# Kernel optimization log

Hardware: AMD Instinct MI355X
Metric: run time of the kernel (lower is better)

## Reference

```python
import jax, jax.numpy as jnp
import numpy as np

RANK = 16
ALPHA = 32
SCALE = ALPHA / RANK


def setup_inputs() -> dict:
    key = jax.random.key(0)
    ks = jax.random.split(key, 4)
    B_, S, D, K = 4, 2048, 4096, 4096
    x = jax.random.normal(ks[0], (B_, S, D), dtype=jnp.float32)
    W = jax.random.normal(ks[1], (K, D), dtype=jnp.float32) * 0.02  # torch Linear weight [out,in]
    bias = jax.random.normal(ks[2], (K,), dtype=jnp.float32) * 0.02
    B = jnp.zeros((D, RANK), dtype=jnp.float32)  # LoRA B init to zeros
    A = jax.random.normal(ks[3], (RANK, K), dtype=jnp.float32)
    return {"x": x, "W": W, "bias": bias, "B": B, "A": A}


def reference(x, W, bias, B, A):
    # base linear: x @ W^T + bias
    base = jnp.einsum("bsd,kd->bsk", x, W) + bias
    # low-rank path: scale * (x @ B) @ A
    lora = SCALE * jnp.einsum("bsr,rk->bsk", jnp.einsum("bsd,dr->bsr", x, B), A)
    return base + lora
```

## Files before the change

### kernel.cpp

```cpp
#include <hip/hip_runtime.h>

typedef unsigned short u16;
typedef __attribute__((ext_vector_type(4))) unsigned short u16x4;
typedef __attribute__((ext_vector_type(8))) unsigned short u16x8;
typedef __attribute__((ext_vector_type(8))) short bf16x8;
typedef __attribute__((ext_vector_type(4))) float f32x4;

#define LORA_SCALE 2.0f

__device__ __forceinline__ u16 f2bf(float f) {
  unsigned u = __builtin_bit_cast(unsigned, f);
  u += 0x7FFFu + ((u >> 16) & 1u);
  return (u16)(u >> 16);
}

#define GLOAD16(g, l) __builtin_amdgcn_global_load_lds(                        \
    (const __attribute__((address_space(1))) void*)(g),                        \
    (__attribute__((address_space(3))) void*)(l), 16, 0, 0)

__global__ __launch_bounds__(256) void make_weff(
    const float* __restrict__ W, const float* __restrict__ B,
    const float* __restrict__ A, u16* __restrict__ Wb)
{
  __shared__ float sA[16][64];
  const int n0 = (blockIdx.x >> 4) * 64;
  const int k0 = (blockIdx.x & 15) * 256;
  const int t  = threadIdx.x;

  {
    const int r = t >> 4;
    const int j = (t & 15) * 4;
    const float4 v = *(const float4*)(A + (size_t)r * 4096 + n0 + j);
    sA[r][j + 0] = LORA_SCALE * v.x;
    sA[r][j + 1] = LORA_SCALE * v.y;
    sA[r][j + 2] = LORA_SCALE * v.z;
    sA[r][j + 3] = LORA_SCALE * v.w;
  }
  __syncthreads();

  const int tn = t >> 6;
  const int tk = t & 63;

  float bv[64];
  const float4* pb = (const float4*)(B + (size_t)(k0 + tk * 4) * 16);
#pragma unroll
  for (int q = 0; q < 16; ++q) {
    float4 v = pb[q];
    bv[q * 4 + 0] = v.x; bv[q * 4 + 1] = v.y;
    bv[q * 4 + 2] = v.z; bv[q * 4 + 3] = v.w;
  }

  for (int i = 0; i < 16; ++i) {
    const int n = n0 + tn * 16 + i;
    const float4 w4 = *(const float4*)(W + (size_t)n * 4096 + k0 + tk * 4);
    float acc[4] = {w4.x, w4.y, w4.z, w4.w};
#pragma unroll
    for (int j = 0; j < 4; ++j)
#pragma unroll
      for (int r = 0; r < 16; ++r)
        acc[j] += bv[j * 16 + r] * sA[r][tn * 16 + i];
    u16x4 o;
    o[0] = f2bf(acc[0]); o[1] = f2bf(acc[1]);
    o[2] = f2bf(acc[2]); o[3] = f2bf(acc[3]);
    *(u16x4*)(Wb + (size_t)n * 4096 + k0 + tk * 4) = o;
  }
}

__global__ __launch_bounds__(256) void cvt_x_kernel(
    const float* __restrict__ x, u16* __restrict__ xb, long n)
{
  long i0 = ((long)blockIdx.x * blockDim.x + threadIdx.x) * 8;
  long stride = (long)gridDim.x * blockDim.x * 8;
  for (long i = i0; i < n; i += stride) {
    float4 a = *(const float4*)(x + i);
    float4 b = *(const float4*)(x + i + 4);
    u16x8 o;
    o[0] = f2bf(a.x); o[1] = f2bf(a.y); o[2] = f2bf(a.z); o[3] = f2bf(a.w);
    o[4] = f2bf(b.x); o[5] = f2bf(b.y); o[6] = f2bf(b.z); o[7] = f2bf(b.w);
    *(u16x8*)(xb + i) = o;
  }
}

__global__ __launch_bounds__(512, 2) void gemm256(
    const u16* __restrict__ Xb, const u16* __restrict__ Wb,
    const float* __restrict__ bias, float* __restrict__ out)
{
  constexpr int K = 4096, N = 4096;
  constexpr int NT = K / 32;
  __shared__ char lds[3 * 32768];

  const int t = threadIdx.x;
  const int w = t >> 6, l = t & 63;
  const int wave_m = w >> 2, wave_n = w & 3;

  const int bid = blockIdx.x;
  const int swz = (bid & 7) * 64 + (bid >> 3);
  const int tm = swz >> 4, tn = swz & 15;
  const int m0 = tm * 256, n0 = tn * 256;

  const int lrow = l >> 2;
  const int lch  = ((l & 3) ^ ((l >> 3) & 3)) * 8;
  const u16* gAs = Xb + (size_t)(m0 + w * 16 + lrow) * K + lch;
  const u16* gBs = Wb + (size_t)(n0 + w * 16 + lrow) * K + lch;
  char* ldsw = lds + w * 1024;

#define STAGE_A(tt, bb) do {                                                   \
    GLOAD16(gAs + (size_t)(tt) * 32,                  ldsw + (bb) * 32768);    \
    GLOAD16(gAs + (size_t)(tt) * 32 + 128 * (size_t)K, ldsw + (bb) * 32768 + 8192); \
  } while (0)
#define STAGE_B(tt, bb) do {                                                   \
    GLOAD16(gBs + (size_t)(tt) * 32,                  ldsw + (bb) * 32768 + 16384); \
    GLOAD16(gBs + (size_t)(tt) * 32 + 128 * (size_t)K, ldsw + (bb) * 32768 + 16384 + 8192); \
  } while (0)

  const int fr = l & 15, fq = l >> 4;
  const int coff = (fq ^ ((fr >> 1) & 3)) << 4;
  const char* pa0 = lds + (wave_m * 128 + fr) * 64 + coff;
  const char* pb0 = lds + 16384 + (wave_n * 64 + fr) * 64 + coff;

  f32x4 acc[8][4];
#pragma unroll
  for (int i = 0; i < 8; ++i)
#pragma unroll
    for (int j = 0; j < 4; ++j) acc[i][j] = (f32x4){0.f, 0.f, 0.f, 0.f};

  STAGE_A(0, 0); STAGE_B(0, 0);
  STAGE_A(1, 1); STAGE_B(1, 1);
  asm volatile("s_waitcnt vmcnt(4)" ::: "memory");
  __builtin_amdgcn_s_barrier();

  int b = 0;
  for (int tt = 0; tt < NT; ++tt) {
    const char* pa = pa0 + b * 32768;
    const char* pb = pb0 + b * 32768;
    const int bs = (b == 2) ? 0 : b + 1;
    const int b2 = (b >= 1) ? b - 1 : 2;

    bf16x8 bf[4], af[4];
#pragma unroll
    for (int nj = 0; nj < 4; ++nj)
      bf[nj] = *(const bf16x8*)(pb + nj * 1024);
#pragma unroll
    for (int mi = 0; mi < 4; ++mi)
      af[mi] = *(const bf16x8*)(pa + mi * 1024);
    if (tt + 2 < NT) STAGE_A(tt + 2, b2);
    __builtin_amdgcn_s_setprio(1);
#pragma unroll
    for (int mi = 0; mi < 4; ++mi)
#pragma unroll
      for (int nj = 0; nj < 4; ++nj)
        acc[mi][nj] = __builtin_amdgcn_mfma_f32_16x16x32_bf16(
            af[mi], bf[nj], acc[mi][nj], 0, 0, 0);
    __builtin_amdgcn_s_setprio(0);

#pragma unroll
    for (int mi = 0; mi < 4; ++mi)
      af[mi] = *(const bf16x8*)(pa + 4096 + mi * 1024);
    if (tt + 2 < NT) STAGE_B(tt + 2, b2);
    __builtin_amdgcn_s_setprio(1);
#pragma unroll
    for (int mi = 0; mi < 4; ++mi)
#pragma unroll
      for (int nj = 0; nj < 4; ++nj)
        acc[4 + mi][nj] = __builtin_amdgcn_mfma_f32_16x16x32_bf16(
            af[mi], bf[nj], acc[4 + mi][nj], 0, 0, 0);
    __builtin_amdgcn_s_setprio(0);

    if (tt + 2 < NT) { asm volatile("s_waitcnt vmcnt(4)" ::: "memory"); }
    else             { asm volatile("s_waitcnt vmcnt(0)" ::: "memory"); }
    __builtin_amdgcn_s_barrier();

    b = bs;
  }

  float bvals[4];
#pragma unroll
  for (int nj = 0; nj < 4; ++nj)
    bvals[nj] = bias[n0 + wave_n * 64 + nj * 16 + fr];

#pragma unroll
  for (int ph = 0; ph < 2; ++ph)
#pragma unroll
    for (int mi = 0; mi < 4; ++mi)
#pragma unroll
      for (int i = 0; i < 4; ++i) {
        const int m = m0 + wave_m * 128 + ph * 64 + mi * 16 + fq * 4 + i;
        float* orow = out + (size_t)m * N + n0 + wave_n * 64 + fr;
#pragma unroll
        for (int nj = 0; nj < 4; ++nj)
          orow[nj * 16] = acc[ph * 4 + mi][nj][i] + bvals[nj];
      }
}

extern "C" void kernel_launch(void* const* d_in, const int* in_sizes, int n_in,
                              void* d_out, int out_size, void* d_ws, size_t ws_size,
                              hipStream_t stream) {
  const float* x    = (const float*)d_in[0];
  const float* W    = (const float*)d_in[1];
  const float* bias = (const float*)d_in[2];
  const float* B    = (const float*)d_in[3];
  const float* A    = (const float*)d_in[4];
  float* out = (float*)d_out;

  u16* Xb = (u16*)d_ws;
  u16* Wb = Xb + (size_t)8192 * 4096;

  make_weff<<<dim3(1024), dim3(256), 0, stream>>>(W, B, A, Wb);
  cvt_x_kernel<<<dim3(2048), dim3(256), 0, stream>>>(x, Xb, (long)8192 * 4096);
  gemm256<<<dim3(512), dim3(512), 0, stream>>>(Xb, Wb, bias, out);
}
```

Baseline: 510.5 us.

## Merge prep kernels into one launch and software-pipeline LDS fragment loads

Folds the weight-merge and x-conversion kernels into a single launch, split by block index, which saves one launch and lets both prep jobs run concurrently. Inside the GEMM loop, the B and first-half A fragments for the next tile are now read from LDS right after the barrier. The second-half A fragment is read at the start of each iteration so the LDS reads overlap MFMA work. This uses more registers in the GEMM and could lower occupancy or cause spills.

```diff
diff --git a/kernel.cpp b/kernel.cpp
--- a/kernel.cpp
+++ b/kernel.cpp
@@ -18,66 +18,66 @@
     (const __attribute__((address_space(1))) void*)(g),                        \
     (__attribute__((address_space(3))) void*)(l), 16, 0, 0)
 
-__global__ __launch_bounds__(256) void make_weff(
+__global__ __launch_bounds__(256) void prep(
     const float* __restrict__ W, const float* __restrict__ B,
-    const float* __restrict__ A, u16* __restrict__ Wb)
-{
-  __shared__ float sA[16][64];
-  const int n0 = (blockIdx.x >> 4) * 64;
-  const int k0 = (blockIdx.x & 15) * 256;
-  const int t  = threadIdx.x;
-
-  {
-    const int r = t >> 4;
-    const int j = (t & 15) * 4;
-    const float4 v = *(const float4*)(A + (size_t)r * 4096 + n0 + j);
-    sA[r][j + 0] = LORA_SCALE * v.x;
-    sA[r][j + 1] = LORA_SCALE * v.y;
-    sA[r][j + 2] = LORA_SCALE * v.z;
-    sA[r][j + 3] = LORA_SCALE * v.w;
-  }
-  __syncthreads();
-
-  const int tn = t >> 6;
-  const int tk = t & 63;
-
-  float bv[64];
-  const float4* pb = (const float4*)(B + (size_t)(k0 + tk * 4) * 16);
-#pragma unroll
-  for (int q = 0; q < 16; ++q) {
-    float4 v = pb[q];
-    bv[q * 4 + 0] = v.x; bv[q * 4 + 1] = v.y;
-    bv[q * 4 + 2] = v.z; bv[q * 4 + 3] = v.w;
-  }
-
-  for (int i = 0; i < 16; ++i) {
-    const int n = n0 + tn * 16 + i;
-    const float4 w4 = *(const float4*)(W + (size_t)n * 4096 + k0 + tk * 4);
-    float acc[4] = {w4.x, w4.y, w4.z, w4.w};
-#pragma unroll
-    for (int j = 0; j < 4; ++j)
-#pragma unroll
-      for (int r = 0; r < 16; ++r)
-        acc[j] += bv[j * 16 + r] * sA[r][tn * 16 + i];
-    u16x4 o;
-    o[0] = f2bf(acc[0]); o[1] = f2bf(acc[1]);
-    o[2] = f2bf(acc[2]); o[3] = f2bf(acc[3]);
-    *(u16x4*)(Wb + (size_t)n * 4096 + k0 + tk * 4) = o;
-  }
-}
-
-__global__ __launch_bounds__(256) void cvt_x_kernel(
+    const float* __restrict__ A, u16* __restrict__ Wb,
     const float* __restrict__ x, u16* __restrict__ xb, long n)
 {
-  long i0 = ((long)blockIdx.x * blockDim.x + threadIdx.x) * 8;
-  long stride = (long)gridDim.x * blockDim.x * 8;
-  for (long i = i0; i < n; i += stride) {
-    float4 a = *(const float4*)(x + i);
-    float4 b = *(const float4*)(x + i + 4);
-    u16x8 o;
-    o[0] = f2bf(a.x); o[1] = f2bf(a.y); o[2] = f2bf(a.z); o[3] = f2bf(a.w);
-    o[4] = f2bf(b.x); o[5] = f2bf(b.y); o[6] = f2bf(b.z); o[7] = f2bf(b.w);
-    *(u16x8*)(xb + i) = o;
+  if (blockIdx.x < 1024) {
+    __shared__ float sA[16][64];
+    const int n0 = ((int)blockIdx.x >> 4) * 64;
+    const int k0 = ((int)blockIdx.x & 15) * 256;
+    const int t  = threadIdx.x;
+
+    {
+      const int r = t >> 4;
+      const int j = (t & 15) * 4;
+      const float4 v = *(const float4*)(A + (size_t)r * 4096 + n0 + j);
+      sA[r][j + 0] = LORA_SCALE * v.x;
+      sA[r][j + 1] = LORA_SCALE * v.y;
+      sA[r][j + 2] = LORA_SCALE * v.z;
+      sA[r][j + 3] = LORA_SCALE * v.w;
+    }
+    __syncthreads();
+
+    const int tn = t >> 6;
+    const int tk = t & 63;
+
+    float bv[64];
+    const float4* pb = (const float4*)(B + (size_t)(k0 + tk * 4) * 16);
+#pragma unroll
+    for (int q = 0; q < 16; ++q) {
+      float4 v = pb[q];
+      bv[q * 4 + 0] = v.x; bv[q * 4 + 1] = v.y;
+      bv[q * 4 + 2] = v.z; bv[q * 4 + 3] = v.w;
+    }
+
+    for (int i = 0; i < 16; ++i) {
+      const int nn = n0 + tn * 16 + i;
+      const float4 w4 = *(const float4*)(W + (size_t)nn * 4096 + k0 + tk * 4);
+      float acc[4] = {w4.x, w4.y, w4.z, w4.w};
+#pragma unroll
+      for (int j = 0; j < 4; ++j)
+#pragma unroll
+        for (int r = 0; r < 16; ++r)
+          acc[j] += bv[j * 16 + r] * sA[r][tn * 16 + i];
+      u16x4 o;
+      o[0] = f2bf(acc[0]); o[1] = f2bf(acc[1]);
+      o[2] = f2bf(acc[2]); o[3] = f2bf(acc[3]);
+      *(u16x4*)(Wb + (size_t)nn * 4096 + k0 + tk * 4) = o;
+    }
+  } else {
+    const long cb = (long)blockIdx.x - 1024;
+    long i0 = (cb * blockDim.x + threadIdx.x) * 8;
+    long stride = (long)2048 * blockDim.x * 8;
+    for (long i = i0; i < n; i += stride) {
+      float4 a = *(const float4*)(x + i);
+      float4 b = *(const float4*)(x + i + 4);
+      u16x8 o;
+      o[0] = f2bf(a.x); o[1] = f2bf(a.y); o[2] = f2bf(a.z); o[3] = f2bf(a.w);
+      o[4] = f2bf(b.x); o[5] = f2bf(b.y); o[6] = f2bf(b.z); o[7] = f2bf(b.w);
+      *(u16x8*)(xb + i) = o;
+    }
   }
 }
 
@@ -129,46 +129,57 @@
   asm volatile("s_waitcnt vmcnt(4)" ::: "memory");
   __builtin_amdgcn_s_barrier();
 
+  bf16x8 bf[4], afA[4];
+#pragma unroll
+  for (int nj = 0; nj < 4; ++nj) bf[nj]  = *(const bf16x8*)(pb0 + nj * 1024);
+#pragma unroll
+  for (int mi = 0; mi < 4; ++mi) afA[mi] = *(const bf16x8*)(pa0 + mi * 1024);
+
   int b = 0;
   for (int tt = 0; tt < NT; ++tt) {
     const char* pa = pa0 + b * 32768;
-    const char* pb = pb0 + b * 32768;
     const int bs = (b == 2) ? 0 : b + 1;
     const int b2 = (b >= 1) ? b - 1 : 2;
 
-    bf16x8 bf[4], af[4];
-#pragma unroll
-    for (int nj = 0; nj < 4; ++nj)
-      bf[nj] = *(const bf16x8*)(pb + nj * 1024);
-#pragma unroll
-    for (int mi = 0; mi < 4; ++mi)
-      af[mi] = *(const bf16x8*)(pa + mi * 1024);
+    bf16x8 afB[4];
+#pragma unroll
+    for (int mi = 0; mi < 4; ++mi)
+      afB[mi] = *(const bf16x8*)(pa + 4096 + mi * 1024);
+
     if (tt + 2 < NT) STAGE_A(tt + 2, b2);
+
     __builtin_amdgcn_s_setprio(1);
 #pragma unroll
     for (int mi = 0; mi < 4; ++mi)
 #pragma unroll
       for (int nj = 0; nj < 4; ++nj)
         acc[mi][nj] = __builtin_amdgcn_mfma_f32_16x16x32_bf16(
-            af[mi], bf[nj], acc[mi][nj], 0, 0, 0);
+            afA[mi], bf[nj], acc[mi][nj], 0, 0, 0);
     __builtin_amdgcn_s_setprio(0);
 
-#pragma unroll
-    for (int mi = 0; mi < 4; ++mi)
-      af[mi] = *(const bf16x8*)(pa + 4096 + mi * 1024);
     if (tt + 2 < NT) STAGE_B(tt + 2, b2);
+
     __builtin_amdgcn_s_setprio(1);
 #pragma unroll
     for (int mi = 0; mi < 4; ++mi)
 #pragma unroll
       for (int nj = 0; nj < 4; ++nj)
         acc[4 + mi][nj] = __builtin_amdgcn_mfma_f32_16x16x32_bf16(
-            af[mi], bf[nj], acc[4 + mi][nj], 0, 0, 0);
+            afB[mi], bf[nj], acc[4 + mi][nj], 0, 0, 0);
     __builtin_amdgcn_s_setprio(0);
 
     if (tt + 2 < NT) { asm volatile("s_waitcnt vmcnt(4)" ::: "memory"); }
     else             { asm volatile("s_waitcnt vmcnt(0)" ::: "memory"); }
     __builtin_amdgcn_s_barrier();
+
+    if (tt + 1 < NT) {
+      const char* pan = pa0 + bs * 32768;
+      const char* pbn = pb0 + bs * 32768;
+#pragma unroll
+      for (int nj = 0; nj < 4; ++nj) bf[nj]  = *(const bf16x8*)(pbn + nj * 1024);
+#pragma unroll
+      for (int mi = 0; mi < 4; ++mi) afA[mi] = *(const bf16x8*)(pan + mi * 1024);
+    }
 
     b = bs;
   }
@@ -205,7 +216,7 @@
   u16* Xb = (u16*)d_ws;
   u16* Wb = Xb + (size_t)8192 * 4096;
 
-  make_weff<<<dim3(1024), dim3(256), 0, stream>>>(W, B, A, Wb);
-  cvt_x_kernel<<<dim3(2048), dim3(256), 0, stream>>>(x, Xb, (long)8192 * 4096);
+  prep<<<dim3(3072), dim3(256), 0, stream>>>(W, B, A, Wb, x, Xb,
+                                             (long)8192 * 4096);
   gemm256<<<dim3(512), dim3(512), 0, stream>>>(Xb, Wb, bias, out);
 }
```

Result: faster. 492.4 us (-3.5%).
